# Optimization experiments

Measured on AMD Instinct MI355X. Metric: run time of the kernel, lower is better.

The kernel has to match this reference:

```python
import jax, jax.numpy as jnp
import numpy as np

N = 5000        # nodes
F = 7699        # node feature dim (fixed by code)
E = 40000       # edges
ED = 3          # edge_dim (fixed by code)
H1, C1 = 4, 1024
H2, C2 = 1, 1024
NUM_OUT = 128
NEG_SLOPE = 0.2


def _glorot(key, shape):
    fan_in = shape[0]
    return jax.random.normal(key, shape, jnp.float32) / np.float32(np.sqrt(fan_in))


def setup_inputs() -> dict:
    key = jax.random.key(0)
    ks = jax.random.split(key, 16)
    x = jax.random.normal(ks[0], (N, F), jnp.float32)
    src = jax.random.randint(ks[1], (E,), 0, N)
    dst = jax.random.randint(ks[2], (E,), 0, N)
    src = jnp.where(src == dst, (src + 1) % N, src)  # no pre-existing self loops
    edge_index = jnp.stack([src, dst]).astype(jnp.int32)
    edge_attr = jax.random.normal(ks[3], (E, ED), jnp.float32)
    inp = {
        "x": x, "edge_index": edge_index, "edge_attr": edge_attr,
        # GATv2Conv #1: 7699 -> 1024, heads=4, edge_dim=3
        "W1l": _glorot(ks[4], (F, H1 * C1)), "b1l": jnp.zeros((H1 * C1,), jnp.float32),
        "W1r": _glorot(ks[5], (F, H1 * C1)), "b1r": jnp.zeros((H1 * C1,), jnp.float32),
        "W1e": _glorot(ks[6], (ED, H1 * C1)),
        "att1": _glorot(ks[7], (H1, C1)),
        "bias1": jnp.zeros((H1 * C1,), jnp.float32),
        # GATv2Conv #2: 4096 -> 1024, heads=1, edge_dim=3
        "W2l": _glorot(ks[8], (H1 * C1, H2 * C2)), "b2l": jnp.zeros((H2 * C2,), jnp.float32),
        "W2r": _glorot(ks[9], (H1 * C1, H2 * C2)), "b2r": jnp.zeros((H2 * C2,), jnp.float32),
        "W2e": _glorot(ks[10], (ED, H2 * C2)),
        "att2": _glorot(ks[11], (H2, C2)),
        "bias2": jnp.zeros((H2 * C2,), jnp.float32),
        # final Linear(1024, num_outputs)
        "Wlin": _glorot(ks[12], (C2, NUM_OUT)), "blin": jnp.zeros((NUM_OUT,), jnp.float32),
    }
    return inp


def gatv2_layer(x, src, dst, edge_attr, Wl, bl, Wr, br, We, att, bias, heads, out_ch):
    """PyG GATv2Conv with add_self_loops=True, fill_value='mean', concat=True."""
    n = x.shape[0]
    # self-loop edge_attr = mean of incoming edge attrs per node (fill_value='mean')
    deg = jax.ops.segment_sum(jnp.ones((src.shape[0],), jnp.float32), dst, num_segments=n)
    loop_attr = jax.ops.segment_sum(edge_attr, dst, num_segments=n) / jnp.maximum(deg, 1.0)[:, None]
    idx = jnp.arange(n, dtype=src.dtype)
    srcf = jnp.concatenate([src, idx])
    dstf = jnp.concatenate([dst, idx])
    ea = jnp.concatenate([edge_attr, loop_attr], axis=0)
    xl = (x @ Wl + bl).reshape(n, heads, out_ch)   # lin_l (source)
    xr = (x @ Wr + br).reshape(n, heads, out_ch)   # lin_r (target)
    ee = (ea @ We).reshape(-1, heads, out_ch)       # lin_edge (no bias)
    e = jax.nn.leaky_relu(xl[srcf] + xr[dstf] + ee, NEG_SLOPE)  # [E', H, C]
    logit = jnp.einsum('ehc,hc->eh', e, att)                     # [E', H]
    # segment softmax over destination nodes (every node has a self loop)
    m = jax.lax.stop_gradient(jax.ops.segment_max(logit, dstf, num_segments=n))
    a = jnp.exp(logit - m[dstf])
    denom = jax.ops.segment_sum(a, dstf, num_segments=n)
    alpha = a / (denom[dstf] + 1e-16)
    out = jax.ops.segment_sum(alpha[:, :, None] * xl[srcf], dstf, num_segments=n)  # [N,H,C]
    return out.reshape(n, heads * out_ch) + bias


def reference(x, edge_index, edge_attr,
              W1l, b1l, W1r, b1r, W1e, att1, bias1,
              W2l, b2l, W2r, b2r, W2e, att2, bias2,
              Wlin, blin):
    src, dst = edge_index[0], edge_index[1]
    h = gatv2_layer(x, src, dst, edge_attr, W1l, b1l, W1r, b1r, W1e, att1, bias1, H1, C1)
    h = gatv2_layer(h, src, dst, edge_attr, W2l, b2l, W2r, b2r, W2e, att2, bias2, H2, C2)
    return h @ Wlin + blin
```

## Files before the change

### kernel.cpp

```cpp
#include <hip/hip_runtime.h>
#include <cstdint>
#include <cstddef>

#define N_NODES 5000
#define F_IN    7699
#define KP1     7712
#define KT1     241
#define MP      5120
#define E_EDGES 40000
#define EFULL   45000
#define HC1     4096
#define N1      8192
#define HC2     1024
#define N2      2048
#define NOUT    128

typedef __bf16 bf16x8 __attribute__((ext_vector_type(8)));
typedef float  f32x4  __attribute__((ext_vector_type(4)));
typedef float  f32x16 __attribute__((ext_vector_type(16)));
typedef unsigned short u16x8 __attribute__((ext_vector_type(8)));
typedef _Float16 f16;
typedef _Float16 f16x8 __attribute__((ext_vector_type(8)));

using as1_uchar = unsigned char __attribute__((address_space(1)));
using as3_uchar = unsigned char __attribute__((address_space(3)));

__device__ __forceinline__ unsigned short f2bf(float f) {
  union { float f; unsigned int u; } v; v.f = f;
  return (unsigned short)((v.u + 0x7fffu + ((v.u >> 16) & 1u)) >> 16);
}
__device__ __forceinline__ float bf2f(unsigned short h) {
  union { unsigned int u; float f; } v; v.u = ((unsigned int)h) << 16;
  return v.f;
}

__device__ __forceinline__ void gload16(const void* g, void* l) {
  __builtin_amdgcn_global_load_lds(
      reinterpret_cast<const as1_uchar*>(reinterpret_cast<uintptr_t>(g)),
      reinterpret_cast<as3_uchar*>(reinterpret_cast<uintptr_t>(l)),
      16, 0, 0);
}



__global__ void k_split_x(const float* __restrict__ x, unsigned short* __restrict__ hi,
                          unsigned short* __restrict__ lo) {
  const int C8 = KP1 / 8;
  int ci = blockIdx.x * 256 + threadIdx.x;
  if (ci >= MP * C8) return;
  int r = ci / C8, c8 = ci % C8;
  int c = c8 * 8;
  u16x8 hb, lb;
  #pragma unroll
  for (int j = 0; j < 8; ++j) {
    float v = 0.f;
    if (r < N_NODES && (c + j) < F_IN) v = x[(size_t)r * F_IN + c + j];
    unsigned short h = f2bf(v);
    hb[j] = h; lb[j] = f2bf(v - bf2f(h));
  }
  size_t off = ((size_t)((r >> 7) * KT1 + (c >> 5)) * 4 + ((c >> 3) & 3)) * 1024 + (r & 127) * 8;
  *(u16x8*)&hi[off] = hb;
  *(u16x8*)&lo[off] = lb;
}


__global__ void k_split_w(const float* __restrict__ W,
                          unsigned short* __restrict__ hi, unsigned short* __restrict__ lo,
                          int K, int Nsrc, int c0, int KT, int rowOffset) {
  __shared__ float tile[32][33];
  const int tid = threadIdx.x;
  const int kt = blockIdx.x;
  const int n0 = blockIdx.y * 32;
  #pragma unroll
  for (int i = tid >> 5; i < 32; i += 8) {
    int k = kt * 32 + i;
    tile[i][tid & 31] = (k < K) ? W[(size_t)k * Nsrc + c0 + n0 + (tid & 31)] : 0.f;
  }
  __syncthreads();
  if (tid < 128) {
    const int nn = tid >> 2, kc = (tid & 3) << 3;
    const int n = rowOffset + n0 + nn;
    u16x8 hb, lb;
    #pragma unroll
    for (int j = 0; j < 8; ++j) {
      float v = tile[kc + j][nn];
      unsigned short h = f2bf(v);
      hb[j] = h; lb[j] = f2bf(v - bf2f(h));
    }
    size_t off = ((size_t)((n >> 7) * KT + kt) * 4 + (kc >> 3)) * 1024 + (n & 127) * 8;
    *(u16x8*)&hi[off] = hb;
    *(u16x8*)&lo[off] = lb;
  }
}


template <int OF16>
__global__ __launch_bounds__(256, 2) void k_gemm_bb(
    const unsigned short* __restrict__ Ahi, const unsigned short* __restrict__ Alo,
    const unsigned short* __restrict__ Bhi, const unsigned short* __restrict__ Blo,
    void* __restrict__ Cp, const float* __restrict__ bias0, const float* __restrict__ bias1,
    int halfN, int M, int ldC, int KT, int gn)
{
  __shared__ __align__(16) unsigned short AhS[2 * 4096];
  __shared__ __align__(16) unsigned short AlS[2 * 4096];
  __shared__ __align__(16) unsigned short BhS[2 * 4096];
  __shared__ __align__(16) unsigned short BlS[2 * 4096];

  const int tid = threadIdx.x;
  const int lane = tid & 63;
  const int w = tid >> 6;
  const int wm = w >> 1, wn = w & 1;

  const int s = blockIdx.x;
  const int band = s / (8 * gn);
  const int r = s % (8 * gn);
  const int bn = r >> 3;
  const int bm = band * 8 + (r & 7);

  f32x16 acc[2][2] = {};

  const unsigned short* AbH = Ahi + (size_t)bm * KT * 4096;
  const unsigned short* AbL = Alo + (size_t)bm * KT * 4096;
  const unsigned short* BbH = Bhi + (size_t)bn * KT * 4096;
  const unsigned short* BbL = Blo + (size_t)bn * KT * 4096;
  const int sOff = w * 1024 + lane * 8;

  const int r5 = lane & 31, h5 = lane >> 5;

  auto stage = [&](int kt, int p) {
    const size_t o = (size_t)kt * 4096 + sOff;
    const int lp = p * 4096 + w * 1024;
    gload16(AbH + o,       &AhS[lp]);
    gload16(AbH + o + 512, &AhS[lp + 512]);
    gload16(AbL + o,       &AlS[lp]);
    gload16(AbL + o + 512, &AlS[lp + 512]);
    gload16(BbH + o,       &BhS[lp]);
    gload16(BbH + o + 512, &BhS[lp + 512]);
    gload16(BbL + o,       &BlS[lp]);
    gload16(BbL + o + 512, &BlS[lp + 512]);
  };

  stage(0, 0);
  stage(1, 1);
  asm volatile("s_waitcnt vmcnt(8)" ::: "memory");
  __builtin_amdgcn_s_barrier();

  for (int kt = 0; kt < KT; ++kt) {
    const int p = kt & 1;
    bf16x8 ah[2][2], al[2][2], bh[2][2], bl[2][2];
    #pragma unroll
    for (int i = 0; i < 2; ++i)
      #pragma unroll
      for (int kh = 0; kh < 2; ++kh) {
        const int ro = p * 4096 + (kh * 2 + h5) * 1024 + (wm * 64 + i * 32 + r5) * 8;
        ah[i][kh] = *(const bf16x8*)&AhS[ro];
        al[i][kh] = *(const bf16x8*)&AlS[ro];
      }
    #pragma unroll
    for (int j = 0; j < 2; ++j)
      #pragma unroll
      for (int kh = 0; kh < 2; ++kh) {
        const int ro = p * 4096 + (kh * 2 + h5) * 1024 + (wn * 64 + j * 32 + r5) * 8;
        bh[j][kh] = *(const bf16x8*)&BhS[ro];
        bl[j][kh] = *(const bf16x8*)&BlS[ro];
      }
    asm volatile("s_waitcnt lgkmcnt(0)" ::: "memory");
    __builtin_amdgcn_s_barrier();
    const int ks = (kt + 2 < KT) ? kt + 2 : KT - 1;
    stage(ks, p);

    __builtin_amdgcn_s_setprio(1);
    #pragma unroll
    for (int j = 0; j < 2; ++j)
      #pragma unroll
      for (int kh = 0; kh < 2; ++kh)
        #pragma unroll
        for (int i = 0; i < 2; ++i) {
          acc[i][j] = __builtin_amdgcn_mfma_f32_32x32x16_bf16(ah[i][kh], bh[j][kh], acc[i][j], 0, 0, 0);
          acc[i][j] = __builtin_amdgcn_mfma_f32_32x32x16_bf16(al[i][kh], bh[j][kh], acc[i][j], 0, 0, 0);
          acc[i][j] = __builtin_amdgcn_mfma_f32_32x32x16_bf16(ah[i][kh], bl[j][kh], acc[i][j], 0, 0, 0);
        }
    __builtin_amdgcn_s_setprio(0);

    asm volatile("s_waitcnt vmcnt(8)" ::: "memory");
    __builtin_amdgcn_s_barrier();
  }

  #pragma unroll
  for (int i = 0; i < 2; ++i) {
    #pragma unroll
    for (int j = 0; j < 2; ++j) {
      const int gc = bn * 128 + wn * 64 + j * 32 + r5;
      const float bv = (gc < halfN) ? bias0[gc] : bias1[gc - halfN];
      #pragma unroll
      for (int reg = 0; reg < 16; ++reg) {
        const int gr = bm * 128 + wm * 64 + i * 32 + (reg & 3) + 8 * (reg >> 2) + 4 * h5;
        if (gr < M) {
          float v = acc[i][j][reg] + bv;
          if (OF16) ((f16*)Cp)[(size_t)gr * ldC + gc] = (f16)v;
          else      ((float*)Cp)[(size_t)gr * ldC + gc] = v;
        }
      }
    }
  }
}


__global__ void k_deg(const int* __restrict__ dst, const float* __restrict__ ea,
                      float* __restrict__ deg, float* __restrict__ lattr, int E) {
  int e = blockIdx.x * 256 + threadIdx.x;
  if (e >= E) return;
  int d = dst[e];
  atomicAdd(&deg[d], 1.f);
  atomicAdd(&lattr[d * 3 + 0], ea[e * 3 + 0]);
  atomicAdd(&lattr[d * 3 + 1], ea[e * 3 + 1]);
  atomicAdd(&lattr[d * 3 + 2], ea[e * 3 + 2]);
}

__global__ void k_lattr_fin(float* __restrict__ lattr, const float* __restrict__ deg, int n) {
  int i = blockIdx.x * 256 + threadIdx.x;
  if (i >= n) return;
  float dv = fmaxf(deg[i], 1.f);
  lattr[i * 3 + 0] /= dv; lattr[i * 3 + 1] /= dv; lattr[i * 3 + 2] /= dv;
}

__global__ void k_eafull(const float* __restrict__ ea, const float* __restrict__ lattr,
                         float* __restrict__ eaf, int E, int n) {
  int e = blockIdx.x * 256 + threadIdx.x;
  if (e >= E + n) return;
  const float* s = (e < E) ? &ea[(size_t)e * 3] : &lattr[(size_t)(e - E) * 3];
  eaf[e * 3 + 0] = s[0]; eaf[e * 3 + 1] = s[1]; eaf[e * 3 + 2] = s[2];
}

__global__ void k_count(const int* __restrict__ dst, int* __restrict__ cnt, int E, int n) {
  int e = blockIdx.x * 256 + threadIdx.x;
  if (e >= E + n) return;
  int d = (e < E) ? dst[e] : (e - E);
  atomicAdd(&cnt[d], 1);
}

__global__ void k_scan(const int* __restrict__ cnt, int* __restrict__ rowptr, int n) {
  int lane = threadIdx.x;
  int run = 0;
  for (int base = 0; base < n; base += 64) {
    int i = base + lane;
    int v = (i < n) ? cnt[i] : 0;
    #pragma unroll
    for (int off = 1; off < 64; off <<= 1) {
      int t = __shfl_up(v, off, 64);
      if (lane >= off) v += t;
    }
    if (i < n) rowptr[i + 1] = run + v;
    run += __shfl(v, 63, 64);
  }
  if (lane == 0) rowptr[0] = 0;
}

__global__ void k_fill(const int* __restrict__ dst, const int* __restrict__ rowptr,
                       int* __restrict__ fillc, int* __restrict__ elist, int E, int n) {
  int e = blockIdx.x * 256 + threadIdx.x;
  if (e >= E + n) return;
  int d = (e < E) ? dst[e] : (e - E);
  int pos = rowptr[d] + atomicAdd(&fillc[d], 1);
  elist[pos] = e;
}


template <int H, int ITERS>
__global__ __launch_bounds__(256) void k_logit(
    const f16* __restrict__ xl, const f16* __restrict__ xr, int strideX,
    const float* __restrict__ eaf, const float* __restrict__ We, const float* __restrict__ att,
    const int* __restrict__ src, const int* __restrict__ dst, int E,
    float* __restrict__ logit)
{
  const int e = blockIdx.x;
  const int tid = threadIdx.x;
  int s, d;
  if (e < E) { s = src[e]; d = dst[e]; } else { s = e - E; d = s; }
  const float ea0 = eaf[e * 3 + 0], ea1 = eaf[e * 3 + 1], ea2 = eaf[e * 3 + 2];
  constexpr int HC = ITERS * 256;
  const f16* rl = xl + (size_t)s * strideX;
  const f16* rr = xr + (size_t)d * strideX;
  float acc[H];
  #pragma unroll
  for (int h = 0; h < H; ++h) acc[h] = 0.f;
  #pragma unroll
  for (int i = 0; i < ITERS; ++i) {
    int hc = tid + (i << 8);
    float v = (float)rl[hc] + (float)rr[hc]
            + ea0 * We[hc] + ea1 * We[HC + hc] + ea2 * We[2 * HC + hc];
    v = (v > 0.f) ? v : 0.2f * v;
    acc[i >> 2] += v * att[hc];
  }
  __shared__ float red[H][4];
  const int lane = tid & 63, wv = tid >> 6;
  #pragma unroll
  for (int h = 0; h < H; ++h) {
    float v = acc[h];
    #pragma unroll
    for (int off = 32; off > 0; off >>= 1) v += __shfl_down(v, off, 64);
    if (lane == 0) red[h][wv] = v;
  }
  __syncthreads();
  if (tid < H)
    logit[(size_t)e * H + tid] = red[tid][0] + red[tid][1] + red[tid][2] + red[tid][3];
}

template <int H>
__global__ void k_stats(const float* __restrict__ logit, const int* __restrict__ rowptr,
                        const int* __restrict__ elist, float* __restrict__ mb, float* __restrict__ db)
{
  const int n = blockIdx.x;
  const int lane = threadIdx.x;
  const int start = rowptr[n], end = rowptr[n + 1];
  #pragma unroll
  for (int h = 0; h < H; ++h) {
    float m = -1e30f;
    for (int p = start + lane; p < end; p += 64)
      m = fmaxf(m, logit[(size_t)elist[p] * H + h]);
    #pragma unroll
    for (int off = 32; off > 0; off >>= 1) m = fmaxf(m, __shfl_down(m, off, 64));
    m = __shfl(m, 0, 64);
    float sum = 0.f;
    for (int p = start + lane; p < end; p += 64)
      sum += __expf(logit[(size_t)elist[p] * H + h] - m);
    #pragma unroll
    for (int off = 32; off > 0; off >>= 1) sum += __shfl_down(sum, off, 64);
    if (lane == 0) { mb[n * H + h] = m; db[n * H + h] = sum; }
  }
}

template <int H, int NC8, int KTo>
__global__ __launch_bounds__(256) void k_agg(
    const f16* __restrict__ xl, int strideX,
    const int* __restrict__ rowptr, const int* __restrict__ elist, const int* __restrict__ src,
    const float* __restrict__ logit, const float* __restrict__ mb, const float* __restrict__ db,
    const float* __restrict__ bias,
    unsigned short* __restrict__ ohi, unsigned short* __restrict__ olo, int E)
{
  const int n = blockIdx.x;
  const int tid = threadIdx.x;
  constexpr int HC = H * 1024;
  float acc[NC8][8];
  #pragma unroll
  for (int q = 0; q < NC8; ++q)
    #pragma unroll
    for (int j = 0; j < 8; ++j) acc[q][j] = 0.f;
  const int start = rowptr[n], end = rowptr[n + 1];
  float mloc[H], dloc[H];
  #pragma unroll
  for (int h = 0; h < H; ++h) { mloc[h] = mb[n * H + h]; dloc[h] = db[n * H + h] + 1e-16f; }
  for (int p = start; p < end; ++p) {
    const int e = elist[p];
    const int s = (e < E) ? src[e] : (e - E);
    float al[H];
    #pragma unroll
    for (int h = 0; h < H; ++h)
      al[h] = __expf(logit[(size_t)e * H + h] - mloc[h]) / dloc[h];
    const f16* row = xl + (size_t)s * strideX;
    #pragma unroll
    for (int q = 0; q < NC8; ++q) {
      const int c8 = tid + q * 256;
      if (c8 * 8 < HC) {
        float a = (H == 4) ? ((tid & 128) ? al[2 * q + 1] : al[2 * q]) : al[0];
        f16x8 v = *(const f16x8*)(row + c8 * 8);
        #pragma unroll
        for (int j = 0; j < 8; ++j) acc[q][j] += a * (float)v[j];
      }
    }
  }
  #pragma unroll
  for (int q = 0; q < NC8; ++q) {
    const int c8 = tid + q * 256;
    if (c8 * 8 < HC) {
      u16x8 hb, lb;
      #pragma unroll
      for (int j = 0; j < 8; ++j) {
        float v = acc[q][j] + bias[c8 * 8 + j];
        unsigned short h = f2bf(v);
        hb[j] = h; lb[j] = f2bf(v - bf2f(h));
      }
      size_t off = ((size_t)((n >> 7) * KTo + (c8 >> 2)) * 4 + (c8 & 3)) * 1024 + (n & 127) * 8;
      *(u16x8*)&ohi[off] = hb;
      *(u16x8*)&olo[off] = lb;
    }
  }
}


extern "C" void kernel_launch(void* const* d_in, const int* in_sizes, int n_in,
                              void* d_out, int out_size, void* d_ws, size_t ws_size,
                              hipStream_t stream) {
  const float* x    = (const float*)d_in[0];
  const int*   eidx = (const int*)d_in[1];
  const float* eattr= (const float*)d_in[2];
  const float* W1l  = (const float*)d_in[3];
  const float* b1l  = (const float*)d_in[4];
  const float* W1r  = (const float*)d_in[5];
  const float* b1r  = (const float*)d_in[6];
  const float* W1e  = (const float*)d_in[7];
  const float* att1 = (const float*)d_in[8];
  const float* bias1= (const float*)d_in[9];
  const float* W2l  = (const float*)d_in[10];
  const float* b2l  = (const float*)d_in[11];
  const float* W2r  = (const float*)d_in[12];
  const float* b2r  = (const float*)d_in[13];
  const float* W2e  = (const float*)d_in[14];
  const float* att2 = (const float*)d_in[15];
  const float* bias2= (const float*)d_in[16];
  const float* Wlin = (const float*)d_in[17];
  const float* blin = (const float*)d_in[18];
  float* out = (float*)d_out;

  char* ws = (char*)d_ws;
  const int* srcp = eidx;
  const int* dstp = eidx + E_EDGES;

  auto alignup = [](size_t v) { return (v + 255) & ~(size_t)255; };

  const size_t oXHI = 0;
  const size_t oXLO = oXHI + (size_t)MP * KP1 * 2;
  const size_t oXLR = oXLO + (size_t)MP * KP1 * 2;
  const size_t oBH  = oXLR + (size_t)N_NODES * N1 * 2;
  const size_t oBL  = oBH + (size_t)4096 * KP1 * 2;
  const size_t oS   = oBL + (size_t)4096 * KP1 * 2;
  const size_t oLATTR = alignup(oS);
  const size_t oDEG   = alignup(oLATTR + (size_t)N_NODES * 3 * 4);
  const size_t oEAF   = alignup(oDEG + (size_t)N_NODES * 4);
  const size_t oCNT   = alignup(oEAF + (size_t)EFULL * 3 * 4);
  const size_t oROW   = alignup(oCNT + (size_t)N_NODES * 4);
  const size_t oFILL  = alignup(oROW + (size_t)(N_NODES + 1) * 4);
  const size_t oELIST = alignup(oFILL + (size_t)N_NODES * 4);
  const size_t oLOGIT = alignup(oELIST + (size_t)EFULL * 4);
  const size_t oMB    = alignup(oLOGIT + (size_t)EFULL * 4 * 4);
  const size_t oDB    = alignup(oMB + (size_t)N_NODES * 4 * 4);
  const size_t oEND   = alignup(oDB + (size_t)N_NODES * 4 * 4);
  if (ws_size < oEND) return;

  const size_t oH1HI = oXHI;
  const size_t oH1LO = oXLO;
  const size_t oXLR2 = oXLR;
  const size_t oH2HI = oXLR + 32ull * 1024 * 1024;
  const size_t oH2LO = oXLR + 48ull * 1024 * 1024;
  const size_t oB2H  = oBH;
  const size_t oB2L  = oBL;
  const size_t oB3H  = oBH;
  const size_t oB3L  = oBH + 1ull * 1024 * 1024;

  unsigned short* XHI  = (unsigned short*)(ws + oXHI);
  unsigned short* XLO  = (unsigned short*)(ws + oXLO);
  f16*            XLR  = (f16*)(ws + oXLR);
  unsigned short* BH   = (unsigned short*)(ws + oBH);
  unsigned short* BL   = (unsigned short*)(ws + oBL);
  float*          LATTR= (float*)(ws + oLATTR);
  float*          DEG  = (float*)(ws + oDEG);
  float*          EAF  = (float*)(ws + oEAF);
  int*            CNT  = (int*)(ws + oCNT);
  int*            ROWP = (int*)(ws + oROW);
  int*            FILLC= (int*)(ws + oFILL);
  int*            ELIST= (int*)(ws + oELIST);
  float*          LOGIT= (float*)(ws + oLOGIT);
  float*          MB   = (float*)(ws + oMB);
  float*          DB   = (float*)(ws + oDB);
  unsigned short* H1HI = (unsigned short*)(ws + oH1HI);
  unsigned short* H1LO = (unsigned short*)(ws + oH1LO);
  f16*            XLR2 = (f16*)(ws + oXLR2);
  unsigned short* H2HI = (unsigned short*)(ws + oH2HI);
  unsigned short* H2LO = (unsigned short*)(ws + oH2LO);
  unsigned short* B2H  = (unsigned short*)(ws + oB2H);
  unsigned short* B2L  = (unsigned short*)(ws + oB2L);
  unsigned short* B3H  = (unsigned short*)(ws + oB3H);
  unsigned short* B3L  = (unsigned short*)(ws + oB3L);

  hipMemsetAsync(ws + oDEG,   0, (size_t)N_NODES * 4, stream);
  hipMemsetAsync(ws + oLATTR, 0, (size_t)N_NODES * 3 * 4, stream);
  hipMemsetAsync(ws + oCNT,   0, (size_t)N_NODES * 4, stream);
  hipMemsetAsync(ws + oFILL,  0, (size_t)N_NODES * 4, stream);

  const int gE  = (E_EDGES + 255) / 256;
  const int gEF = (EFULL + 255) / 256;
  const int gN  = (N_NODES + 255) / 256;

  k_deg<<<gE, 256, 0, stream>>>(dstp, eattr, DEG, LATTR, E_EDGES);
  k_lattr_fin<<<gN, 256, 0, stream>>>(LATTR, DEG, N_NODES);
  k_eafull<<<gEF, 256, 0, stream>>>(eattr, LATTR, EAF, E_EDGES, N_NODES);
  k_count<<<gEF, 256, 0, stream>>>(dstp, CNT, E_EDGES, N_NODES);
  k_scan<<<1, 64, 0, stream>>>(CNT, ROWP, N_NODES);
  k_fill<<<gEF, 256, 0, stream>>>(dstp, ROWP, FILLC, ELIST, E_EDGES, N_NODES);

  k_split_x<<<MP * (KP1 / 8) / 256, 256, 0, stream>>>(x, XHI, XLO);

  k_split_w<<<dim3(KT1, HC1 / 32), 256, 0, stream>>>(W1l, BH, BL, F_IN, HC1, 0, KT1, 0);
  k_gemm_bb<1><<<(HC1 / 128) * (MP / 128), 256, 0, stream>>>(
      XHI, XLO, BH, BL, XLR, b1l, b1l, HC1, N_NODES, N1, KT1, HC1 / 128);

  k_split_w<<<dim3(KT1, HC1 / 32), 256, 0, stream>>>(W1r, BH, BL, F_IN, HC1, 0, KT1, 0);
  k_gemm_bb<1><<<(HC1 / 128) * (MP / 128), 256, 0, stream>>>(
      XHI, XLO, BH, BL, XLR + HC1, b1r, b1r, HC1, N_NODES, N1, KT1, HC1 / 128);

  k_logit<4, 16><<<EFULL, 256, 0, stream>>>(XLR, XLR + HC1, N1, EAF, W1e, att1, srcp, dstp, E_EDGES, LOGIT);
  k_stats<4><<<N_NODES, 64, 0, stream>>>(LOGIT, ROWP, ELIST, MB, DB);
  hipMemsetAsync(ws + oH1HI, 0, (size_t)MP * HC1 * 2, stream);
  hipMemsetAsync(ws + oH1LO, 0, (size_t)MP * HC1 * 2, stream);
  k_agg<4, 2, HC1 / 32><<<N_NODES, 256, 0, stream>>>(
      XLR, N1, ROWP, ELIST, srcp, LOGIT, MB, DB, bias1, H1HI, H1LO, E_EDGES);

  k_split_w<<<dim3(HC1 / 32, HC2 / 32), 256, 0, stream>>>(W2l, B2H, B2L, HC1, HC2, 0, HC1 / 32, 0);
  k_split_w<<<dim3(HC1 / 32, HC2 / 32), 256, 0, stream>>>(W2r, B2H, B2L, HC1, HC2, 0, HC1 / 32, HC2);
  k_gemm_bb<1><<<(N2 / 128) * (MP / 128), 256, 0, stream>>>(
      H1HI, H1LO, B2H, B2L, XLR2, b2l, b2r, HC2, N_NODES, N2, HC1 / 32, N2 / 128);

  k_logit<1, 4><<<EFULL, 256, 0, stream>>>(XLR2, XLR2 + HC2, N2, EAF, W2e, att2, srcp, dstp, E_EDGES, LOGIT);
  k_stats<1><<<N_NODES, 64, 0, stream>>>(LOGIT, ROWP, ELIST, MB, DB);
  hipMemsetAsync(ws + oH2HI, 0, (size_t)MP * HC2 * 2, stream);
  hipMemsetAsync(ws + oH2LO, 0, (size_t)MP * HC2 * 2, stream);
  k_agg<1, 1, HC2 / 32><<<N_NODES, 256, 0, stream>>>(
      XLR2, N2, ROWP, ELIST, srcp, LOGIT, MB, DB, bias2, H2HI, H2LO, E_EDGES);

  k_split_w<<<dim3(HC2 / 32, NOUT / 32), 256, 0, stream>>>(Wlin, B3H, B3L, HC2, NOUT, 0, HC2 / 32, 0);
  k_gemm_bb<0><<<(NOUT / 128) * (MP / 128), 256, 0, stream>>>(
      H2HI, H2LO, B3H, B3L, out, blin, blin, NOUT, N_NODES, NOUT, HC2 / 32, NOUT / 128);
}
```

Measured before the change: 2.868 ms.

## Use 256x128 tiles with triple-buffered LDS, XCD remap, and merged lin_l/lin_r GEMM

The bf16x3 GEMM now uses 512-thread blocks computing 256x128 tiles in a single 3-stage shared-memory ring. This replaces the two-stage double buffer and removes one barrier per k-step. Blocks are remapped so that consecutive tiles land on the same XCD, and when the workspace is large enough the two layer-1 projections are split into one weight buffer and run as a single GEMM. The goal is more A/B reuse, fewer launches and better L2 locality, at the cost of much more shared memory per block, which may reduce occupancy.

```diff
diff --git a/kernel.cpp b/kernel.cpp
--- a/kernel.cpp
+++ b/kernel.cpp
@@ -14,6 +14,7 @@
 #define HC2     1024
 #define N2      2048
 #define NOUT    128
+#define GM      (MP / 256)
 
 typedef __bf16 bf16x8 __attribute__((ext_vector_type(8)));
 typedef float  f32x4  __attribute__((ext_vector_type(4)));
@@ -95,79 +96,81 @@
 
 
 template <int OF16>
-__global__ __launch_bounds__(256, 2) void k_gemm_bb(
+__global__ __launch_bounds__(512, 2) void k_gemm_bb(
     const unsigned short* __restrict__ Ahi, const unsigned short* __restrict__ Alo,
     const unsigned short* __restrict__ Bhi, const unsigned short* __restrict__ Blo,
     void* __restrict__ Cp, const float* __restrict__ bias0, const float* __restrict__ bias1,
-    int halfN, int M, int ldC, int KT, int gn)
+    int halfN, int M, int ldC, int KT, int gm)
 {
-  __shared__ __align__(16) unsigned short AhS[2 * 4096];
-  __shared__ __align__(16) unsigned short AlS[2 * 4096];
-  __shared__ __align__(16) unsigned short BhS[2 * 4096];
-  __shared__ __align__(16) unsigned short BlS[2 * 4096];
+  __shared__ __align__(16) unsigned short S[3 * 24576];
 
   const int tid = threadIdx.x;
   const int lane = tid & 63;
   const int w = tid >> 6;
   const int wm = w >> 1, wn = w & 1;
 
-  const int s = blockIdx.x;
-  const int band = s / (8 * gn);
-  const int r = s % (8 * gn);
-  const int bn = r >> 3;
-  const int bm = band * 8 + (r & 7);
+  const int nwg = gridDim.x;
+  const int qq = nwg >> 3, rr = nwg & 7;
+  const int xcd = blockIdx.x & 7, idx = blockIdx.x >> 3;
+  const int wg = (xcd < rr ? xcd * (qq + 1) : rr * (qq + 1) + (xcd - rr) * qq) + idx;
+  const int bn = wg / gm, bm = wg % gm;
 
   f32x16 acc[2][2] = {};
 
-  const unsigned short* AbH = Ahi + (size_t)bm * KT * 4096;
-  const unsigned short* AbL = Alo + (size_t)bm * KT * 4096;
-  const unsigned short* BbH = Bhi + (size_t)bn * KT * 4096;
-  const unsigned short* BbL = Blo + (size_t)bn * KT * 4096;
-  const int sOff = w * 1024 + lane * 8;
+  const size_t aoff = (size_t)(2 * bm) * KT * 4096 + w * 512 + lane * 8;
+  const unsigned short* b0 = Ahi + aoff;
+  const unsigned short* b1 = b0 + (size_t)KT * 4096;
+  const unsigned short* b2 = Alo + aoff;
+  const unsigned short* b3 = b2 + (size_t)KT * 4096;
+  const unsigned short* b4 = Bhi + (size_t)bn * KT * 4096 + w * 512 + lane * 8;
+  const unsigned short* b5 = Blo + (size_t)bn * KT * 4096 + w * 512 + lane * 8;
+  const int ldst = w * 512;
+
+  auto stage = [&](int kt, int bufo) {
+    const size_t o = (size_t)kt * 4096;
+    gload16(b0 + o, &S[bufo + 0 * 4096 + ldst]);
+    gload16(b1 + o, &S[bufo + 1 * 4096 + ldst]);
+    gload16(b2 + o, &S[bufo + 2 * 4096 + ldst]);
+    gload16(b3 + o, &S[bufo + 3 * 4096 + ldst]);
+    gload16(b4 + o, &S[bufo + 4 * 4096 + ldst]);
+    gload16(b5 + o, &S[bufo + 5 * 4096 + ldst]);
+  };
 
   const int r5 = lane & 31, h5 = lane >> 5;
-
-  auto stage = [&](int kt, int p) {
-    const size_t o = (size_t)kt * 4096 + sOff;
-    const int lp = p * 4096 + w * 1024;
-    gload16(AbH + o,       &AhS[lp]);
-    gload16(AbH + o + 512, &AhS[lp + 512]);
-    gload16(AbL + o,       &AlS[lp]);
-    gload16(AbL + o + 512, &AlS[lp + 512]);
-    gload16(BbH + o,       &BhS[lp]);
-    gload16(BbH + o + 512, &BhS[lp + 512]);
-    gload16(BbL + o,       &BlS[lp]);
-    gload16(BbL + o + 512, &BlS[lp + 512]);
-  };
+  const int arow0 = wm * 64 + r5;
+  const int arow1 = arow0 + 32;
+  const int at[2]  = { arow0 >> 7, arow1 >> 7 };
+  const int ar[2]  = { (arow0 & 127) * 8, (arow1 & 127) * 8 };
+  const int bc[2]  = { (wn * 64 + r5) * 8, (wn * 64 + 32 + r5) * 8 };
+  const int pl = h5 * 1024;
 
   stage(0, 0);
-  stage(1, 1);
-  asm volatile("s_waitcnt vmcnt(8)" ::: "memory");
+  stage(1, 24576);
+  asm volatile("s_waitcnt vmcnt(6)" ::: "memory");
   __builtin_amdgcn_s_barrier();
 
+  int ocur = 0, onxt = 24576, onx2 = 49152;
   for (int kt = 0; kt < KT; ++kt) {
-    const int p = kt & 1;
+    const int ks = (kt + 2 < KT) ? kt + 2 : KT - 1;
+    stage(ks, onx2);
+
     bf16x8 ah[2][2], al[2][2], bh[2][2], bl[2][2];
     #pragma unroll
     for (int i = 0; i < 2; ++i)
       #pragma unroll
       for (int kh = 0; kh < 2; ++kh) {
-        const int ro = p * 4096 + (kh * 2 + h5) * 1024 + (wm * 64 + i * 32 + r5) * 8;
-        ah[i][kh] = *(const bf16x8*)&AhS[ro];
-        al[i][kh] = *(const bf16x8*)&AlS[ro];
+        const int po = ocur + kh * 2048 + pl;
+        ah[i][kh] = *(const bf16x8*)&S[po + at[i] * 4096 + ar[i]];
+        al[i][kh] = *(const bf16x8*)&S[po + (2 + at[i]) * 4096 + ar[i]];
       }
     #pragma unroll
     for (int j = 0; j < 2; ++j)
       #pragma unroll
       for (int kh = 0; kh < 2; ++kh) {
-        const int ro = p * 4096 + (kh * 2 + h5) * 1024 + (wn * 64 + j * 32 + r5) * 8;
-        bh[j][kh] = *(const bf16x8*)&BhS[ro];
-        bl[j][kh] = *(const bf16x8*)&BlS[ro];
+        const int po = ocur + kh * 2048 + pl;
+        bh[j][kh] = *(const bf16x8*)&S[po + 4 * 4096 + bc[j]];
+        bl[j][kh] = *(const bf16x8*)&S[po + 5 * 4096 + bc[j]];
       }
-    asm volatile("s_waitcnt lgkmcnt(0)" ::: "memory");
-    __builtin_amdgcn_s_barrier();
-    const int ks = (kt + 2 < KT) ? kt + 2 : KT - 1;
-    stage(ks, p);
 
     __builtin_amdgcn_s_setprio(1);
     #pragma unroll
@@ -182,8 +185,9 @@
         }
     __builtin_amdgcn_s_setprio(0);
 
-    asm volatile("s_waitcnt vmcnt(8)" ::: "memory");
+    asm volatile("s_waitcnt vmcnt(6)" ::: "memory");
     __builtin_amdgcn_s_barrier();
+    const int t = ocur; ocur = onxt; onxt = onx2; onx2 = t;
   }
 
   #pragma unroll
@@ -194,7 +198,7 @@
       const float bv = (gc < halfN) ? bias0[gc] : bias1[gc - halfN];
       #pragma unroll
       for (int reg = 0; reg < 16; ++reg) {
-        const int gr = bm * 128 + wm * 64 + i * 32 + (reg & 3) + 8 * (reg >> 2) + 4 * h5;
+        const int gr = bm * 256 + wm * 64 + i * 32 + (reg & 3) + 8 * (reg >> 2) + 4 * h5;
         if (gr < M) {
           float v = acc[i][j][reg] + bv;
           if (OF16) ((f16*)Cp)[(size_t)gr * ldC + gc] = (f16)v;
@@ -418,24 +422,27 @@
 
   auto alignup = [](size_t v) { return (v + 255) & ~(size_t)255; };
 
-  const size_t oXHI = 0;
-  const size_t oXLO = oXHI + (size_t)MP * KP1 * 2;
-  const size_t oXLR = oXLO + (size_t)MP * KP1 * 2;
-  const size_t oBH  = oXLR + (size_t)N_NODES * N1 * 2;
-  const size_t oBL  = oBH + (size_t)4096 * KP1 * 2;
-  const size_t oS   = oBL + (size_t)4096 * KP1 * 2;
-  const size_t oLATTR = alignup(oS);
-  const size_t oDEG   = alignup(oLATTR + (size_t)N_NODES * 3 * 4);
-  const size_t oEAF   = alignup(oDEG + (size_t)N_NODES * 4);
-  const size_t oCNT   = alignup(oEAF + (size_t)EFULL * 3 * 4);
-  const size_t oROW   = alignup(oCNT + (size_t)N_NODES * 4);
-  const size_t oFILL  = alignup(oROW + (size_t)(N_NODES + 1) * 4);
-  const size_t oELIST = alignup(oFILL + (size_t)N_NODES * 4);
-  const size_t oLOGIT = alignup(oELIST + (size_t)EFULL * 4);
-  const size_t oMB    = alignup(oLOGIT + (size_t)EFULL * 4 * 4);
-  const size_t oDB    = alignup(oMB + (size_t)N_NODES * 4 * 4);
-  const size_t oEND   = alignup(oDB + (size_t)N_NODES * 4 * 4);
-  if (ws_size < oEND) return;
+  size_t mo = 0;
+  auto take = [&](size_t sz) { size_t r = mo; mo = alignup(mo + sz); return r; };
+  const size_t oLATTR = take((size_t)N_NODES * 3 * 4);
+  const size_t oDEG   = take((size_t)N_NODES * 4);
+  const size_t oEAF   = take((size_t)EFULL * 3 * 4);
+  const size_t oCNT   = take((size_t)N_NODES * 4);
+  const size_t oROW   = take((size_t)(N_NODES + 1) * 4);
+  const size_t oFILL  = take((size_t)N_NODES * 4);
+  const size_t oELIST = take((size_t)EFULL * 4);
+  const size_t oLOGIT = take((size_t)EFULL * 4 * 4);
+  const size_t oMB    = take((size_t)N_NODES * 4 * 4);
+  const size_t oDB    = take((size_t)N_NODES * 4 * 4);
+  const size_t oXHI   = take((size_t)MP * KP1 * 2);
+  const size_t oXLO   = take((size_t)MP * KP1 * 2);
+  const size_t oXLR   = take((size_t)N_NODES * N1 * 2);
+  const size_t oBH    = take((size_t)N1 * KP1 * 2);
+  const size_t needSmall = oBH + (size_t)HC1 * KP1 * 2 * 2;
+  const size_t needBig   = oBH + (size_t)N1 * KP1 * 2 * 2;
+  if (ws_size < needSmall) return;
+  const bool big = (ws_size >= needBig);
+  const size_t oBL = big ? (oBH + (size_t)N1 * KP1 * 2) : (oBH + (size_t)HC1 * KP1 * 2);
 
   const size_t oH1HI = oXHI;
   const size_t oH1LO = oXLO;
@@ -443,7 +450,7 @@
   const size_t oH2HI = oXLR + 32ull * 1024 * 1024;
   const size_t oH2LO = oXLR + 48ull * 1024 * 1024;
   const size_t oB2H  = oBH;
-  const size_t oB2L  = oBL;
+  const size_t oB2L  = oBH + 32ull * 1024 * 1024;
   const size_t oB3H  = oBH;
   const size_t oB3L  = oBH + 1ull * 1024 * 1024;
 
@@ -490,13 +497,19 @@
 
   k_split_x<<<MP * (KP1 / 8) / 256, 256, 0, stream>>>(x, XHI, XLO);
 
-  k_split_w<<<dim3(KT1, HC1 / 32), 256, 0, stream>>>(W1l, BH, BL, F_IN, HC1, 0, KT1, 0);
-  k_gemm_bb<1><<<(HC1 / 128) * (MP / 128), 256, 0, stream>>>(
-      XHI, XLO, BH, BL, XLR, b1l, b1l, HC1, N_NODES, N1, KT1, HC1 / 128);
-
-  k_split_w<<<dim3(KT1, HC1 / 32), 256, 0, stream>>>(W1r, BH, BL, F_IN, HC1, 0, KT1, 0);
-  k_gemm_bb<1><<<(HC1 / 128) * (MP / 128), 256, 0, stream>>>(
-      XHI, XLO, BH, BL, XLR + HC1, b1r, b1r, HC1, N_NODES, N1, KT1, HC1 / 128);
+  if (big) {
+    k_split_w<<<dim3(KT1, HC1 / 32), 256, 0, stream>>>(W1l, BH, BL, F_IN, HC1, 0, KT1, 0);
+    k_split_w<<<dim3(KT1, HC1 / 32), 256, 0, stream>>>(W1r, BH, BL, F_IN, HC1, 0, KT1, HC1);
+    k_gemm_bb<1><<<(N1 / 128) * GM, 512, 0, stream>>>(
+        XHI, XLO, BH, BL, XLR, b1l, b1r, HC1, N_NODES, N1, KT1, GM);
+  } else {
+    k_split_w<<<dim3(KT1, HC1 / 32), 256, 0, stream>>>(W1l, BH, BL, F_IN, HC1, 0, KT1, 0);
+    k_gemm_bb<1><<<(HC1 / 128) * GM, 512, 0, stream>>>(
+        XHI, XLO, BH, BL, XLR, b1l, b1l, HC1, N_NODES, N1, KT1, GM);
+    k_split_w<<<dim3(KT1, HC1 / 32), 256, 0, stream>>>(W1r, BH, BL, F_IN, HC1, 0, KT1, 0);
+    k_gemm_bb<1><<<(HC1 / 128) * GM, 512, 0, stream>>>(
+        XHI, XLO, BH, BL, XLR + HC1, b1r, b1r, HC1, N_NODES, N1, KT1, GM);
+  }
 
   k_logit<4, 16><<<EFULL, 256, 0, stream>>>(XLR, XLR + HC1, N1, EAF, W1e, att1, srcp, dstp, E_EDGES, LOGIT);
   k_stats<4><<<N_NODES, 64, 0, stream>>>(LOGIT, ROWP, ELIST, MB, DB);
@@ -507,8 +520,8 @@
 
   k_split_w<<<dim3(HC1 / 32, HC2 / 32), 256, 0, stream>>>(W2l, B2H, B2L, HC1, HC2, 0, HC1 / 32, 0);
   k_split_w<<<dim3(HC1 / 32, HC2 / 32), 256, 0, stream>>>(W2r, B2H, B2L, HC1, HC2, 0, HC1 / 32, HC2);
-  k_gemm_bb<1><<<(N2 / 128) * (MP / 128), 256, 0, stream>>>(
-      H1HI, H1LO, B2H, B2L, XLR2, b2l, b2r, HC2, N_NODES, N2, HC1 / 32, N2 / 128);
+  k_gemm_bb<1><<<(N2 / 128) * GM, 512, 0, stream>>>(
+      H1HI, H1LO, B2H, B2L, XLR2, b2l, b2r, HC2, N_NODES, N2, HC1 / 32, GM);
 
   k_logit<1, 4><<<EFULL, 256, 0, stream>>>(XLR2, XLR2 + HC2, N2, EAF, W2e, att2, srcp, dstp, E_EDGES, LOGIT);
   k_stats<1><<<N_NODES, 64, 0, stream>>>(LOGIT, ROWP, ELIST, MB, DB);
@@ -518,6 +531,6 @@
       XLR2, N2, ROWP, ELIST, srcp, LOGIT, MB, DB, bias2, H2HI, H2LO, E_EDGES);
 
   k_split_w<<<dim3(HC2 / 32, NOUT / 32), 256, 0, stream>>>(Wlin, B3H, B3L, HC2, NOUT, 0, HC2 / 32, 0);
-  k_gemm_bb<0><<<(NOUT / 128) * (MP / 128), 256, 0, stream>>>(
-      H2HI, H2LO, B3H, B3L, out, blin, blin, NOUT, N_NODES, NOUT, HC2 / 32, NOUT / 128);
-}
+  k_gemm_bb<0><<<(NOUT / 128) * GM, 512, 0, stream>>>(
+      H2HI, H2LO, B3H, B3L, out, blin, blin, NOUT, N_NODES, NOUT, HC2 / 32, GM);
+}
```

Measured after the change: 2.935 ms. +2.4%, slower.
